# Optimization experiments

Measured on AMD Instinct MI355X. Metric: run time of the kernel, lower is better.

Reference implementation:

```python
import jax, jax.numpy as jnp
import numpy as np

C = 384; H = 32; W = 32; HEADS = 12; HD = C // HEADS; MLP = 1536
KOFF = 5; OFF_RANGE = 2.0


def layer_norm(x, g, b, eps=1e-5):
    mu = jnp.mean(x, axis=-1, keepdims=True)
    var = jnp.mean(jnp.square(x - mu), axis=-1, keepdims=True)
    return (x - mu) * jax.lax.rsqrt(var + eps) * g + b


def depthwise_conv(x, k):
    # x: (B,H,W,C), k: (kh,kw,1,C), SAME padding, groups=C
    return jax.lax.conv_general_dilated(
        x, k, window_strides=(1, 1), padding='SAME',
        dimension_numbers=('NHWC', 'HWIO', 'NHWC'), feature_group_count=C)


def grid_sample_bilinear(img, pos):
    # img: (B,H,W,C); pos: (B,H,W,2) normalized (y,x) in [-1,1], align_corners=True, border clamp
    B, Hh, Ww, Cc = img.shape
    py = (pos[..., 0] + 1.0) * 0.5 * (Hh - 1)
    px = (pos[..., 1] + 1.0) * 0.5 * (Ww - 1)
    y0 = jnp.floor(py); x0 = jnp.floor(px)
    wy = (py - y0)[..., None]; wx = (px - x0)[..., None]
    y0i = jnp.clip(y0.astype(jnp.int32), 0, Hh - 1)
    y1i = jnp.clip(y0i + 1, 0, Hh - 1)
    x0i = jnp.clip(x0.astype(jnp.int32), 0, Ww - 1)
    x1i = jnp.clip(x0i + 1, 0, Ww - 1)
    b = jnp.arange(B)[:, None, None]
    g = lambda yi, xi: img[b, yi, xi]
    return (g(y0i, x0i) * (1 - wy) * (1 - wx) + g(y0i, x1i) * (1 - wy) * wx
            + g(y1i, x0i) * wy * (1 - wx) + g(y1i, x1i) * wy * wx)


def setup_inputs() -> dict:
    key = jax.random.key(0)
    ks = jax.random.split(key, 16)
    n = jax.random.normal
    s = 0.02
    inp = {
        'x': n(ks[0], (16, H * W, C), jnp.float32),
        'ln1_g': jnp.ones((C,), jnp.float32), 'ln1_b': jnp.zeros((C,), jnp.float32),
        'Wq': n(ks[1], (C, C), jnp.float32) * s, 'bq': jnp.zeros((C,), jnp.float32),
        'off_k': n(ks[2], (KOFF, KOFF, 1, C), jnp.float32) * s,
        'off_kb': jnp.zeros((C,), jnp.float32),
        'offln_g': jnp.ones((C,), jnp.float32), 'offln_b': jnp.zeros((C,), jnp.float32),
        'Woff': n(ks[3], (2, C), jnp.float32) * s, 'boff': jnp.zeros((2,), jnp.float32),
        'Wk': n(ks[4], (C, C), jnp.float32) * s, 'bk': jnp.zeros((C,), jnp.float32),
        'Wv': n(ks[5], (C, C), jnp.float32) * s, 'bv': jnp.zeros((C,), jnp.float32),
        'Wo': n(ks[6], (C, C), jnp.float32) * s, 'bo': jnp.zeros((C,), jnp.float32),
        'ln2_g': jnp.ones((C,), jnp.float32), 'ln2_b': jnp.zeros((C,), jnp.float32),
        'W1': n(ks[7], (MLP, C), jnp.float32) * s, 'b1': jnp.zeros((MLP,), jnp.float32),
        'W2': n(ks[8], (C, MLP), jnp.float32) * s, 'b2': jnp.zeros((C,), jnp.float32),
    }
    return inp


def _block(x, ln1_g, ln1_b, Wq, bq, off_k, off_kb, offln_g, offln_b, Woff, boff,
           Wk, bk, Wv, bv, Wo, bo, ln2_g, ln2_b, W1, b1, W2, b2):
    B, N, _ = x.shape
    # --- deformable attention branch ---
    xn = layer_norm(x, ln1_g, ln1_b)
    xi = xn.reshape(B, H, W, C)
    q = xi @ Wq.T + bq                                  # (B,H,W,C)
    # offset network: depthwise conv -> LN -> GELU -> 1x1 conv to 2
    off = depthwise_conv(q, off_k) + off_kb
    off = jax.nn.gelu(layer_norm(off, offln_g, offln_b))
    off = off @ Woff.T + boff                           # (B,H,W,2)
    off_range = jnp.array([OFF_RANGE * 2.0 / H, OFF_RANGE * 2.0 / W], jnp.float32)
    off = jnp.tanh(off) * off_range                     # normalized coord units
    ry = (jnp.arange(H, dtype=jnp.float32) + 0.5) / H * 2.0 - 1.0
    rx = (jnp.arange(W, dtype=jnp.float32) + 0.5) / W * 2.0 - 1.0
    ref = jnp.stack(jnp.meshgrid(ry, rx, indexing='ij'), axis=-1)  # (H,W,2)
    pos = ref[None] + off                               # (B,H,W,2)
    xs = grid_sample_bilinear(xi, pos).reshape(B, N, C)  # sampled keys/values source
    k = xs @ Wk.T + bk
    v = xs @ Wv.T + bv
    qh = q.reshape(B, N, HEADS, HD).transpose(0, 2, 1, 3)
    kh = k.reshape(B, N, HEADS, HD).transpose(0, 2, 1, 3)
    vh = v.reshape(B, N, HEADS, HD).transpose(0, 2, 1, 3)
    attn = jax.nn.softmax(jnp.einsum('bhqd,bhkd->bhqk', qh, kh) * (HD ** -0.5), axis=-1)
    o = jnp.einsum('bhqk,bhkd->bhqd', attn, vh).transpose(0, 2, 1, 3).reshape(B, N, C)
    x = x + (o @ Wo.T + bo)
    # --- MLP branch ---
    y = layer_norm(x, ln2_g, ln2_b)
    y = jax.nn.gelu(y @ W1.T + b1) @ W2.T + b2
    return x + y


def reference(x, ln1_g, ln1_b, Wq, bq, off_k, off_kb, offln_g, offln_b, Woff, boff,
              Wk, bk, Wv, bv, Wo, bo, ln2_g, ln2_b, W1, b1, W2, b2):
    return _block(x, ln1_g, ln1_b, Wq, bq, off_k, off_kb, offln_g, offln_b, Woff, boff,
                  Wk, bk, Wv, bv, Wo, bo, ln2_g, ln2_b, W1, b1, W2, b2)
```

## Files before the change

kernel.cpp:

```cpp
#include <hip/hip_runtime.h>
#include <math.h>

#define DI __device__ __forceinline__

typedef __attribute__((ext_vector_type(8))) short bf16x8;
typedef __attribute__((ext_vector_type(4))) float f32x4;

static constexpr int CC = 384;
static constexpr float QSCALE = 0.17677669529663687f * 1.4426950408889634f;
static constexpr float INVQS  = 1.0f / QSCALE;

DI unsigned short f2bf(float f){
  unsigned u = __float_as_uint(f);
  u += 0x7FFFu + ((u >> 16) & 1u);
  return (unsigned short)(u >> 16);
}
DI float bf2f(unsigned short u){ return __uint_as_float((unsigned)u << 16); }
DI float lo16(unsigned u){ return __uint_as_float(u << 16); }
DI float hi16(unsigned u){ return __uint_as_float(u & 0xFFFF0000u); }
DI float fexp2(float x){ return __builtin_amdgcn_exp2f(x); }
DI float frcp(float x){ return __builtin_amdgcn_rcpf(x); }
DI float tanh_fast(float z){ return 1.f - 2.f*frcp(fexp2(2.8853900817779268f*z) + 1.f); }
DI float gelu_fast(float v){
  float u = v*v;
  float z = 0.7978845608028654f * fmaf(0.044715f*u, v, v);
  return v - v*frcp(fexp2(2.8853900817779268f*z) + 1.f);
}
DI f32x4 mfma16(bf16x8 a, bf16x8 b, f32x4 c){
  return __builtin_amdgcn_mfma_f32_16x16x32_bf16(a, b, c, 0, 0, 0);
}
DI void gload16(const unsigned short* g, unsigned short* l){
  __builtin_amdgcn_global_load_lds(
      (const __attribute__((address_space(1))) unsigned int*)(const void*)g,
      (__attribute__((address_space(3))) unsigned int*)(void*)l, 16, 0, 0);
}

__global__ __launch_bounds__(256) void k_cvt_all(
    const float* __restrict__ wq, const float* __restrict__ wk,
    const float* __restrict__ wv, const float* __restrict__ wo,
    const float* __restrict__ w1, const float* __restrict__ w2,
    const float* __restrict__ ofk,
    unsigned short* __restrict__ dst)
{
  int i4 = (blockIdx.x*256 + threadIdx.x)*4;
  if (i4 >= 1779072) return;
  const float* src; int off;
  if (i4 < 147456){ src = wq; off = i4; }
  else if (i4 < 294912){ src = wk; off = i4 - 147456; }
  else if (i4 < 442368){ src = wv; off = i4 - 294912; }
  else if (i4 < 589824){ src = wo; off = i4 - 442368; }
  else if (i4 < 1179648){ src = w1; off = i4 - 589824; }
  else if (i4 < 1769472){ src = w2; off = i4 - 1179648; }
  else { src = ofk; off = i4 - 1769472; }
  float4 v = *(const float4*)(src + off);
  uint2 o;
  o.x = ((unsigned)f2bf(v.y) << 16) | f2bf(v.x);
  o.y = ((unsigned)f2bf(v.w) << 16) | f2bf(v.z);
  *(uint2*)(dst + i4) = o;
}

template<int BIN>
__global__ __launch_bounds__(256) void k_ln(const float* __restrict__ xf,
    const unsigned short* __restrict__ xb,
    const float* __restrict__ g, const float* __restrict__ b,
    unsigned short* __restrict__ outb)
{
  int row = blockIdx.x*4 + (threadIdx.x >> 6);
  int l = threadIdx.x & 63;
  float v[6]; int ch[6];
  if constexpr (BIN){
    int cA = 4*l, cB = 256 + 2*l;
    ch[0]=cA; ch[1]=cA+1; ch[2]=cA+2; ch[3]=cA+3; ch[4]=cB; ch[5]=cB+1;
    const unsigned short* xp = xb + (size_t)row * CC;
    uint2 u2 = *(const uint2*)(xp + cA);
    unsigned u1 = *(const unsigned*)(xp + cB);
    v[0]=lo16(u2.x); v[1]=hi16(u2.x); v[2]=lo16(u2.y); v[3]=hi16(u2.y);
    v[4]=lo16(u1);   v[5]=hi16(u1);
  } else {
    const float* xp = xf + (size_t)row * CC;
#pragma unroll
    for (int p = 0; p < 6; p++){ ch[p] = l + 64*p; v[p] = xp[ch[p]]; }
  }
  float s = 0.f, s2 = 0.f;
#pragma unroll
  for (int p = 0; p < 6; p++){ s += v[p]; s2 += v[p]*v[p]; }
#pragma unroll
  for (int m = 32; m; m >>= 1){ s += __shfl_xor(s, m); s2 += __shfl_xor(s2, m); }
  float mu = s * (1.f/CC);
  float var = s2 * (1.f/CC) - mu*mu;
  float rs = rsqrtf(var + 1e-5f);
  float o[6];
#pragma unroll
  for (int p = 0; p < 6; p++) o[p] = (v[p] - mu) * rs * g[ch[p]] + b[ch[p]];
  unsigned short* op = outb + (size_t)row*CC;
  if constexpr (BIN){
    uint2 st;
    st.x = ((unsigned)f2bf(o[1]) << 16) | f2bf(o[0]);
    st.y = ((unsigned)f2bf(o[3]) << 16) | f2bf(o[2]);
    *(uint2*)(op + ch[0]) = st;
    *(unsigned*)(op + ch[4]) = ((unsigned)f2bf(o[5]) << 16) | f2bf(o[4]);
  } else {
#pragma unroll
    for (int p = 0; p < 6; p++) op[ch[p]] = f2bf(o[p]);
  }
}

template<int EPI>
__global__ __launch_bounds__(256) void k_gemm64(
    const unsigned short* __restrict__ A, const unsigned short* __restrict__ W,
    const float* __restrict__ bias, const float* __restrict__ bias2,
    const float* __restrict__ res, const unsigned short* __restrict__ resb,
    float* __restrict__ outf, unsigned short* __restrict__ outb,
    unsigned short* __restrict__ outb2, int ntn, int N, int K)
{
  __shared__ unsigned short As[2][2048];
  __shared__ unsigned short Bs[2][4096];
  int bid = blockIdx.x;
  int cpx = gridDim.x >> 3;
  int id = (bid & 7)*cpx + (bid >> 3);
  int bn = (id % ntn) * 128;
  int bm = (id / ntn) * 64;
  int t = threadIdx.x;
  int w = t >> 6, l = t & 63;
  int g = l >> 4, ln = l & 15;
  int wm = w >> 1, wn = w & 1;
  f32x4 acc[2][4];
#pragma unroll
  for (int i = 0; i < 2; i++)
#pragma unroll
    for (int j = 0; j < 4; j++) acc[i][j] = (f32x4){0.f,0.f,0.f,0.f};
  int srow = t >> 2, slot = t & 3;
  int srowB = srow + 64;
  int cb0 = (slot ^ (srow  & 3) ^ ((srow  >> 2) & 3)) * 8;
  int cb1 = (slot ^ (srowB & 3) ^ ((srowB >> 2) & 3)) * 8;
  const unsigned short* Ap  = A + (size_t)(bm + srow)*K + cb0;
  const unsigned short* Wp0 = W + (size_t)(bn + srow)*K + cb0;
  const unsigned short* Wp1 = W + (size_t)(bn + srowB)*K + cb1;
  int NT = K >> 5;
  int wl = w*512;
  gload16(Ap,  &As[0][wl]);
  gload16(Wp0, &Bs[0][wl]);
  gload16(Wp1, &Bs[0][wl + 2048]);
  __syncthreads();
  for (int kt = 0; kt < NT; kt++){
    int cur = kt & 1;
    if (kt + 1 < NT){
      int k0 = (kt + 1) << 5;
      gload16(Ap  + k0, &As[cur ^ 1][wl]);
      gload16(Wp0 + k0, &Bs[cur ^ 1][wl]);
      gload16(Wp1 + k0, &Bs[cur ^ 1][wl + 2048]);
    }
    bf16x8 af[2], bf[4];
#pragma unroll
    for (int mi = 0; mi < 2; mi++){
      int row = wm*32 + mi*16 + ln;
      int sl = g ^ (row & 3) ^ ((row >> 2) & 3);
      af[mi] = *(const bf16x8*)((const char*)As[cur] + row*64 + sl*16);
    }
#pragma unroll
    for (int ni = 0; ni < 4; ni++){
      int row = wn*64 + ni*16 + ln;
      int sl = g ^ (row & 3) ^ ((row >> 2) & 3);
      bf[ni] = *(const bf16x8*)((const char*)Bs[cur] + row*64 + sl*16);
    }
#pragma unroll
    for (int mi = 0; mi < 2; mi++)
#pragma unroll
      for (int ni = 0; ni < 4; ni++)
        acc[mi][ni] = mfma16(af[mi], bf[ni], acc[mi][ni]);
    if (kt + 1 < NT) __syncthreads();
  }
#pragma unroll
  for (int mi = 0; mi < 2; mi++)
#pragma unroll
  for (int ni = 0; ni < 4; ni++){
    int col = bn + wn*64 + ni*16 + ln;
    float bv;
    if constexpr (EPI == 6) bv = col < 384 ? bias[col] : bias2[col - 384];
    else bv = bias[col];
#pragma unroll
    for (int i = 0; i < 4; i++){
      int row = bm + wm*32 + mi*16 + g*4 + i;
      float v = acc[mi][ni][i] + bv;
      if constexpr (EPI == 2){ v += res[(size_t)row*N + col]; outb[(size_t)row*N + col] = f2bf(v); }
      if constexpr (EPI == 7){ v += bf2f(resb[(size_t)row*N + col]); outf[(size_t)row*N + col] = v; }
      if constexpr (EPI == 3) v = gelu_fast(v);
      if constexpr (EPI == 0) outf[(size_t)row*N + col] = v;
      if constexpr (EPI == 1 || EPI == 3) outb[(size_t)row*N + col] = f2bf(v);
      if constexpr (EPI == 5) outb[(size_t)row*N + col] = f2bf(v * QSCALE);
      if constexpr (EPI == 6){
        if (col < 384){
          outb[(size_t)row*384 + col] = f2bf(v);
        } else {
          int c = col - 384;
          int bb = row >> 10, key = row & 1023, h = c >> 5, d = c & 31;
          int k6 = key & 63;
          int phys = (key & ~63) | ((k6 & 15) << 2) | (k6 >> 4);
          outb2[(size_t)(((bb*12 + h) << 5) + d)*1024 + phys] = f2bf(v);
        }
      }
    }
  }
}

__global__ __launch_bounds__(256) void k_mlp1(
    const unsigned short* __restrict__ A, const unsigned short* __restrict__ W,
    const float* __restrict__ bias, unsigned short* __restrict__ outb)
{
  __shared__ unsigned short As[2][4096];
  __shared__ unsigned short Bs[2][4096];
  int bid = blockIdx.x;
  int cpx = gridDim.x >> 3;
  int id = (bid & 7)*cpx + (bid >> 3);
  int bn = (id % 12) * 128;
  int bm = (id / 12) * 128;
  int t = threadIdx.x;
  int w = t >> 6, l = t & 63;
  int g = l >> 4, ln = l & 15;
  int wm = w >> 1, wn = w & 1;
  f32x4 acc[4][4];
#pragma unroll
  for (int i = 0; i < 4; i++)
#pragma unroll
    for (int j = 0; j < 4; j++) acc[i][j] = (f32x4){0.f,0.f,0.f,0.f};
  int srow0 = t >> 2, slot = t & 3;
  int srow1 = srow0 + 64;
  int cb0 = (slot ^ (srow0 & 3) ^ ((srow0 >> 2) & 3)) * 8;
  int cb1 = (slot ^ (srow1 & 3) ^ ((srow1 >> 2) & 3)) * 8;
  const unsigned short* Ap0 = A + (size_t)(bm + srow0)*384 + cb0;
  const unsigned short* Ap1 = A + (size_t)(bm + srow1)*384 + cb1;
  const unsigned short* Wp0 = W + (size_t)(bn + srow0)*384 + cb0;
  const unsigned short* Wp1 = W + (size_t)(bn + srow1)*384 + cb1;
  int wl = w*512;
  gload16(Ap0, &As[0][wl]);
  gload16(Ap1, &As[0][wl + 2048]);
  gload16(Wp0, &Bs[0][wl]);
  gload16(Wp1, &Bs[0][wl + 2048]);
  __syncthreads();
  for (int kt = 0; kt < 12; kt++){
    int cur = kt & 1;
    if (kt < 11){
      int k0 = (kt + 1) << 5;
      gload16(Ap0 + k0, &As[cur ^ 1][wl]);
      gload16(Ap1 + k0, &As[cur ^ 1][wl + 2048]);
      gload16(Wp0 + k0, &Bs[cur ^ 1][wl]);
      gload16(Wp1 + k0, &Bs[cur ^ 1][wl + 2048]);
    }
    bf16x8 af[4], bf[4];
#pragma unroll
    for (int mi = 0; mi < 4; mi++){
      int row = wm*64 + mi*16 + ln;
      int sl = g ^ (row & 3) ^ ((row >> 2) & 3);
      af[mi] = *(const bf16x8*)((const char*)As[cur] + row*64 + sl*16);
    }
#pragma unroll
    for (int ni = 0; ni < 4; ni++){
      int row = wn*64 + ni*16 + ln;
      int sl = g ^ (row & 3) ^ ((row >> 2) & 3);
      bf[ni] = *(const bf16x8*)((const char*)Bs[cur] + row*64 + sl*16);
    }
#pragma unroll
    for (int mi = 0; mi < 4; mi++)
#pragma unroll
      for (int ni = 0; ni < 4; ni++)
        acc[mi][ni] = mfma16(af[mi], bf[ni], acc[mi][ni]);
    if (kt < 11) __syncthreads();
  }
#pragma unroll
  for (int mi = 0; mi < 4; mi++)
#pragma unroll
  for (int ni = 0; ni < 4; ni++){
    int col = bn + wn*64 + ni*16 + ln;
    float bv = bias[col];
#pragma unroll
    for (int i = 0; i < 4; i++){
      int row = bm + wm*64 + mi*16 + g*4 + i;
      float v = gelu_fast(acc[mi][ni][i] + bv);
      outb[(size_t)row*1536 + col] = f2bf(v);
    }
  }
}

__global__ __launch_bounds__(64) void k_offset_sample(
    const unsigned short* __restrict__ qs, const unsigned short* __restrict__ xnb,
    const unsigned short* __restrict__ okb,
    const float* __restrict__ offkb,
    const float* __restrict__ offg, const float* __restrict__ offb,
    const float* __restrict__ Woff, const float* __restrict__ boff,
    unsigned short* __restrict__ xsb)
{
  int blk = blockIdx.x;
  int pix = (blk & 7)*2048 + (blk >> 3);
  int b = pix >> 10, n = pix & 1023;
  int y = n >> 5, x = n & 31;
  int t = threadIdx.x;
  int c8 = (t < 48 ? t : 47) * 8;
  float act = t < 48 ? 1.f : 0.f;
  const unsigned short* qb = qs + (size_t)b*1024*CC;
  int ry[5], rx[5]; unsigned my[5], mx[5];
#pragma unroll
  for (int k = 0; k < 5; k++){
    int yy = y + k - 2, xx = x + k - 2;
    my[k] = (yy >= 0 && yy < 32) ? 0xFFFFFFFFu : 0u;
    mx[k] = (xx >= 0 && xx < 32) ? 0xFFFFFFFFu : 0u;
    int yc = yy < 0 ? 0 : (yy > 31 ? 31 : yy);
    int xc = xx < 0 ? 0 : (xx > 31 ? 31 : xx);
    ry[k] = yc*32*CC; rx[k] = xc*CC;
  }
  float a[8];
#pragma unroll
  for (int j = 0; j < 8; j++) a[j] = 0.f;
#pragma unroll
  for (int ky = 0; ky < 5; ky++)
#pragma unroll
  for (int kx = 0; kx < 5; kx++){
    int tap = ky*5 + kx;
    unsigned m = my[ky] & mx[kx];
    uint4 q4 = *(const uint4*)(qb + ry[ky] + rx[kx] + c8);
    uint4 w4 = *(const uint4*)(okb + tap*CC + c8);
    q4.x &= m; q4.y &= m; q4.z &= m; q4.w &= m;
    a[0] = fmaf(lo16(q4.x), lo16(w4.x), a[0]);
    a[1] = fmaf(hi16(q4.x), hi16(w4.x), a[1]);
    a[2] = fmaf(lo16(q4.y), lo16(w4.y), a[2]);
    a[3] = fmaf(hi16(q4.y), hi16(w4.y), a[3]);
    a[4] = fmaf(lo16(q4.z), lo16(w4.z), a[4]);
    a[5] = fmaf(hi16(q4.z), hi16(w4.z), a[5]);
    a[6] = fmaf(lo16(q4.w), lo16(w4.w), a[6]);
    a[7] = fmaf(hi16(q4.w), hi16(w4.w), a[7]);
  }
  float4 kbA = *(const float4*)(offkb + c8);
  float4 kbB = *(const float4*)(offkb + c8 + 4);
  float c[8];
  c[0] = act * fmaf(a[0], INVQS, kbA.x);
  c[1] = act * fmaf(a[1], INVQS, kbA.y);
  c[2] = act * fmaf(a[2], INVQS, kbA.z);
  c[3] = act * fmaf(a[3], INVQS, kbA.w);
  c[4] = act * fmaf(a[4], INVQS, kbB.x);
  c[5] = act * fmaf(a[5], INVQS, kbB.y);
  c[6] = act * fmaf(a[6], INVQS, kbB.z);
  c[7] = act * fmaf(a[7], INVQS, kbB.w);
  float s = 0.f, s2 = 0.f;
#pragma unroll
  for (int j = 0; j < 8; j++){ s += c[j]; s2 += c[j]*c[j]; }
#pragma unroll
  for (int m2 = 32; m2; m2 >>= 1){ s += __shfl_xor(s, m2); s2 += __shfl_xor(s2, m2); }
  float mu = s * (1.f/CC);
  float var = s2 * (1.f/CC) - mu*mu;
  float rs = rsqrtf(var + 1e-5f);
  float4 gA = *(const float4*)(offg + c8); float4 gB = *(const float4*)(offg + c8 + 4);
  float4 oA = *(const float4*)(offb + c8); float4 oB = *(const float4*)(offb + c8 + 4);
  float4 wA = *(const float4*)(Woff + c8); float4 wB = *(const float4*)(Woff + c8 + 4);
  float4 wC = *(const float4*)(Woff + CC + c8); float4 wD = *(const float4*)(Woff + CC + c8 + 4);
  float gg[8] = {gA.x,gA.y,gA.z,gA.w,gB.x,gB.y,gB.z,gB.w};
  float bb[8] = {oA.x,oA.y,oA.z,oA.w,oB.x,oB.y,oB.z,oB.w};
  float w0[8] = {wA.x,wA.y,wA.z,wA.w,wB.x,wB.y,wB.z,wB.w};
  float w1[8] = {wC.x,wC.y,wC.z,wC.w,wD.x,wD.y,wD.z,wD.w};
  float p0 = 0.f, p1 = 0.f;
#pragma unroll
  for (int j = 0; j < 8; j++){
    float v = gelu_fast((c[j] - mu)*rs*gg[j] + bb[j]) * act;
    p0 = fmaf(v, w0[j], p0);
    p1 = fmaf(v, w1[j], p1);
  }
#pragma unroll
  for (int m2 = 32; m2; m2 >>= 1){ p0 += __shfl_xor(p0, m2); p1 += __shfl_xor(p1, m2); }
  float offy = tanh_fast(p0 + boff[0]) * 0.125f;
  float offx = tanh_fast(p1 + boff[1]) * 0.125f;
  float py = ((y + 0.5f)/16.f - 1.f + offy + 1.f) * 0.5f * 31.f;
  float px = ((x + 0.5f)/16.f - 1.f + offx + 1.f) * 0.5f * 31.f;
  float y0f = floorf(py), x0f = floorf(px);
  float wy = py - y0f, wx = px - x0f;
  int y0 = (int)y0f, x0 = (int)x0f;
  y0 = y0 < 0 ? 0 : (y0 > 31 ? 31 : y0);
  x0 = x0 < 0 ? 0 : (x0 > 31 ? 31 : x0);
  int y1 = y0 + 1 > 31 ? 31 : y0 + 1;
  int x1 = x0 + 1 > 31 ? 31 : x0 + 1;
  const unsigned short* s00 = xnb + (size_t)(b*1024 + y0*32 + x0)*CC + c8;
  const unsigned short* s01 = xnb + (size_t)(b*1024 + y0*32 + x1)*CC + c8;
  const unsigned short* s10 = xnb + (size_t)(b*1024 + y1*32 + x0)*CC + c8;
  const unsigned short* s11 = xnb + (size_t)(b*1024 + y1*32 + x1)*CC + c8;
  float w00 = (1.f-wy)*(1.f-wx), w01 = (1.f-wy)*wx, w10 = wy*(1.f-wx), w11 = wy*wx;
  uint4 A0 = *(const uint4*)s00;
  uint4 A1 = *(const uint4*)s01;
  uint4 A2 = *(const uint4*)s10;
  uint4 A3 = *(const uint4*)s11;
  if (t < 48){
    float r[8];
    r[0] = w00*lo16(A0.x) + w01*lo16(A1.x) + w10*lo16(A2.x) + w11*lo16(A3.x);
    r[1] = w00*hi16(A0.x) + w01*hi16(A1.x) + w10*hi16(A2.x) + w11*hi16(A3.x);
    r[2] = w00*lo16(A0.y) + w01*lo16(A1.y) + w10*lo16(A2.y) + w11*lo16(A3.y);
    r[3] = w00*hi16(A0.y) + w01*hi16(A1.y) + w10*hi16(A2.y) + w11*hi16(A3.y);
    r[4] = w00*lo16(A0.z) + w01*lo16(A1.z) + w10*lo16(A2.z) + w11*lo16(A3.z);
    r[5] = w00*hi16(A0.z) + w01*hi16(A1.z) + w10*hi16(A2.z) + w11*hi16(A3.z);
    r[6] = w00*lo16(A0.w) + w01*lo16(A1.w) + w10*lo16(A2.w) + w11*lo16(A3.w);
    r[7] = w00*hi16(A0.w) + w01*hi16(A1.w) + w10*hi16(A2.w) + w11*hi16(A3.w);
    uint4 st;
    st.x = ((unsigned)f2bf(r[1]) << 16) | f2bf(r[0]);
    st.y = ((unsigned)f2bf(r[3]) << 16) | f2bf(r[2]);
    st.z = ((unsigned)f2bf(r[5]) << 16) | f2bf(r[4]);
    st.w = ((unsigned)f2bf(r[7]) << 16) | f2bf(r[6]);
    *(uint4*)(xsb + (size_t)(b*1024 + n)*CC + c8) = st;
  }
}

__global__ __launch_bounds__(256) void k_attn(
    const unsigned short* __restrict__ qs, const unsigned short* __restrict__ kb,
    const unsigned short* __restrict__ vt, unsigned short* __restrict__ ob)
{
  __shared__ unsigned short Ks[2][64][40];
  __shared__ unsigned short Vs[2][32][72];
  __shared__ unsigned short Ps[4][32][72];
  int blk = blockIdx.x;
  int sw = (blk & 7)*192 + (blk >> 3);
  int qt = sw & 7, h = (sw >> 3) % 12, b = sw / 96;
  int t = threadIdx.x;
  int w = t >> 6, l = t & 63;
  int g = l >> 4, ln = l & 15;
  int q0 = qt*128 + w*32;
  bf16x8 qa[2];
#pragma unroll
  for (int mi = 0; mi < 2; mi++)
    qa[mi] = *(const bf16x8*)&qs[(size_t)(b*1024 + q0 + mi*16 + ln)*CC + h*32 + g*8];
  bf16x8 vones;
#pragma unroll
  for (int j = 0; j < 8; j++) vones[j] = (short)0x3F80;
  f32x4 z = {0.f,0.f,0.f,0.f};
  f32x4 oacc[2][2]; oacc[0][0]=z; oacc[0][1]=z; oacc[1][0]=z; oacc[1][1]=z;
  f32x4 lacc[2]; lacc[0]=z; lacc[1]=z;
  int krow = t >> 2, kc = (t & 3)*8;
  int vdim = t >> 3, vc = (t & 7)*8;
  const unsigned short* kptr = kb + (size_t)(b*1024 + krow)*CC + h*32 + kc;
  const unsigned short* vptr = vt + (size_t)((b*12 + h)*32 + vdim)*1024 + vc;
  {
    uint4 kr = *(const uint4*)kptr;
    uint4 vr = *(const uint4*)vptr;
    *(uint4*)&Ks[0][krow][kc] = kr;
    *(uint4*)&Vs[0][vdim][vc] = vr;
  }
  __syncthreads();
  for (int kt = 0; kt < 16; kt++){
    int cur = kt & 1;
    uint4 kr2, vr2;
    if (kt < 15){
      int k0 = (kt + 1)*64;
      kr2 = *(const uint4*)(kptr + (size_t)k0*CC);
      vr2 = *(const uint4*)(vptr + k0);
    }
    bf16x8 kf[4];
#pragma unroll
    for (int nt = 0; nt < 4; nt++) kf[nt] = *(const bf16x8*)&Ks[cur][nt*16 + ln][g*8];
    f32x4 s[2][4];
    __builtin_amdgcn_s_setprio(1);
#pragma unroll
    for (int mi = 0; mi < 2; mi++)
#pragma unroll
      for (int nt = 0; nt < 4; nt++) s[mi][nt] = mfma16(qa[mi], kf[nt], z);
    __builtin_amdgcn_s_setprio(0);
#pragma unroll
    for (int mi = 0; mi < 2; mi++)
#pragma unroll
      for (int i = 0; i < 4; i++){
        float p0 = fexp2(s[mi][0][i]);
        float p1 = fexp2(s[mi][1][i]);
        float p2 = fexp2(s[mi][2][i]);
        float p3 = fexp2(s[mi][3][i]);
        int prow = mi*16 + g*4 + i;
        uint2 pk;
        pk.x = __builtin_amdgcn_perm(__float_as_uint(p1), __float_as_uint(p0), 0x07060302u);
        pk.y = __builtin_amdgcn_perm(__float_as_uint(p3), __float_as_uint(p2), 0x07060302u);
        *(uint2*)&Ps[w][prow][ln*4] = pk;
      }
    __builtin_amdgcn_s_setprio(1);
#pragma unroll
    for (int k2 = 0; k2 < 2; k2++){
      bf16x8 va[2];
#pragma unroll
      for (int d2 = 0; d2 < 2; d2++) va[d2] = *(const bf16x8*)&Vs[cur][d2*16 + ln][k2*32 + g*8];
#pragma unroll
      for (int mi = 0; mi < 2; mi++){
        bf16x8 pf = *(const bf16x8*)&Ps[w][mi*16 + ln][k2*32 + g*8];
#pragma unroll
        for (int d2 = 0; d2 < 2; d2++) oacc[mi][d2] = mfma16(pf, va[d2], oacc[mi][d2]);
        lacc[mi] = mfma16(pf, vones, lacc[mi]);
      }
    }
    __builtin_amdgcn_s_setprio(0);
    if (kt < 15){
      *(uint4*)&Ks[cur ^ 1][krow][kc] = kr2;
      *(uint4*)&Vs[cur ^ 1][vdim][vc] = vr2;
      __syncthreads();
    }
  }
  float rinv[2][4];
#pragma unroll
  for (int mi = 0; mi < 2; mi++)
#pragma unroll
    for (int i = 0; i < 4; i++) rinv[mi][i] = frcp(lacc[mi][i]);
#pragma unroll
  for (int mi = 0; mi < 2; mi++)
#pragma unroll
  for (int d2 = 0; d2 < 2; d2++)
#pragma unroll
  for (int i = 0; i < 4; i++){
    float v = oacc[mi][d2][i] * rinv[mi][i];
    int row = q0 + mi*16 + g*4 + i;
    ob[(size_t)(b*1024 + row)*CC + h*32 + d2*16 + ln] = f2bf(v);
  }
}

extern "C" void kernel_launch(void* const* d_in, const int* in_sizes, int n_in,
                              void* d_out, int out_size, void* d_ws, size_t ws_size,
                              hipStream_t stream)
{
  (void)in_sizes; (void)n_in; (void)out_size; (void)ws_size;
  const float* x     = (const float*)d_in[0];
  const float* ln1g  = (const float*)d_in[1];
  const float* ln1b  = (const float*)d_in[2];
  const float* Wq    = (const float*)d_in[3];
  const float* bq    = (const float*)d_in[4];
  const float* offk  = (const float*)d_in[5];
  const float* offkb = (const float*)d_in[6];
  const float* offg  = (const float*)d_in[7];
  const float* offb  = (const float*)d_in[8];
  const float* Woff  = (const float*)d_in[9];
  const float* boff  = (const float*)d_in[10];
  const float* Wk    = (const float*)d_in[11];
  const float* bk    = (const float*)d_in[12];
  const float* Wv    = (const float*)d_in[13];
  const float* bv    = (const float*)d_in[14];
  const float* Wo    = (const float*)d_in[15];
  const float* bo    = (const float*)d_in[16];
  const float* ln2g  = (const float*)d_in[17];
  const float* ln2b  = (const float*)d_in[18];
  const float* W1    = (const float*)d_in[19];
  const float* b1    = (const float*)d_in[20];
  const float* W2    = (const float*)d_in[21];
  const float* b2    = (const float*)d_in[22];

  char* ws = (char*)d_ws;
  unsigned short* X2B = (unsigned short*)ws;
  unsigned short* XSB = (unsigned short*)(ws + 25165824);
  unsigned short* KB  = (unsigned short*)(ws + 37748736);
  unsigned short* VT  = (unsigned short*)(ws + 50331648);
  unsigned short* OB  = (unsigned short*)(ws + 62914560);
  unsigned short* XNB = (unsigned short*)(ws + 75497472);
  unsigned short* QSB = (unsigned short*)(ws + 88080384);
  unsigned short* YB  = QSB;
  unsigned short* HB  = (unsigned short*)(ws + 25165824);
  unsigned short* WQB = (unsigned short*)(ws + 100663296);
  unsigned short* WKB = WQB + 147456;
  unsigned short* WOB = WKB + 294912;
  unsigned short* W1B = WOB + 147456;
  unsigned short* W2B = W1B + 589824;
  unsigned short* OKB = W2B + 589824;

  k_cvt_all<<<1738, 256, 0, stream>>>(Wq, Wk, Wv, Wo, W1, W2, offk, WQB);
  k_ln<0><<<4096, 256, 0, stream>>>(x, nullptr, ln1g, ln1b, XNB);
  k_gemm64<5><<<768, 256, 0, stream>>>(XNB, WQB, bq, nullptr, nullptr, nullptr, nullptr, QSB, nullptr, 3, 384, 384);
  k_offset_sample<<<16384, 64, 0, stream>>>(QSB, XNB, OKB, offkb, offg, offb, Woff, boff, XSB);
  k_gemm64<6><<<1536, 256, 0, stream>>>(XSB, WKB, bk, bv, nullptr, nullptr, nullptr, KB, VT, 6, 768, 384);
  k_attn<<<1536, 256, 0, stream>>>(QSB, KB, VT, OB);
  k_gemm64<2><<<768, 256, 0, stream>>>(OB, WOB, bo, nullptr, x, nullptr, nullptr, X2B, nullptr, 3, 384, 384);
  k_ln<1><<<4096, 256, 0, stream>>>(nullptr, X2B, ln2g, ln2b, YB);
  k_mlp1<<<1536, 256, 0, stream>>>(YB, W1B, b1, HB);
  k_gemm64<7><<<768, 256, 0, stream>>>(HB, W2B, b2, nullptr, nullptr, X2B, (float*)d_out, nullptr, nullptr, 3, 384, 1536);
}
```

Baseline: 240.3 us.

## Keep attention probabilities in registers via transposed QK^T MFMA

The score MFMA now runs with operands swapped, computing S^T. Each lane's accumulator then already matches the A-operand layout of the PV MFMA, so the exponentiated probabilities are packed to bf16 in registers instead of round-tripping through a per-warp shared-memory P buffer. The V-transpose permutation written by the QKV projection epilogue is changed to match the new key ordering within each 64-key tile. This removes LDS stores and loads and their latency, and frees shared memory, at the cost of tying correctness to that key permutation.

```diff
diff --git a/kernel.cpp b/kernel.cpp
--- a/kernel.cpp
+++ b/kernel.cpp
@@ -33,6 +33,9 @@
   __builtin_amdgcn_global_load_lds(
       (const __attribute__((address_space(1))) unsigned int*)(const void*)g,
       (__attribute__((address_space(3))) unsigned int*)(void*)l, 16, 0, 0);
+}
+DI unsigned packbf(float pa, float pb){
+  return __builtin_amdgcn_perm(__float_as_uint(pb), __float_as_uint(pa), 0x07060302u);
 }
 
 __global__ __launch_bounds__(256) void k_cvt_all(
@@ -195,7 +198,7 @@
           int c = col - 384;
           int bb = row >> 10, key = row & 1023, h = c >> 5, d = c & 31;
           int k6 = key & 63;
-          int phys = (key & ~63) | ((k6 & 15) << 2) | (k6 >> 4);
+          int phys = (key & ~63) | (k6 & 0x23) | ((k6 & 0xC) << 1) | ((k6 & 0x10) >> 2);
           outb2[(size_t)(((bb*12 + h) << 5) + d)*1024 + phys] = f2bf(v);
         }
       }
@@ -409,7 +412,6 @@
 {
   __shared__ unsigned short Ks[2][64][40];
   __shared__ unsigned short Vs[2][32][72];
-  __shared__ unsigned short Ps[4][32][72];
   int blk = blockIdx.x;
   int sw = (blk & 7)*192 + (blk >> 3);
   int qt = sw & 7, h = (sw >> 3) % 12, b = sw / 96;
@@ -449,27 +451,30 @@
     bf16x8 kf[4];
 #pragma unroll
     for (int nt = 0; nt < 4; nt++) kf[nt] = *(const bf16x8*)&Ks[cur][nt*16 + ln][g*8];
-    f32x4 s[2][4];
+    f32x4 st[2][4];
     __builtin_amdgcn_s_setprio(1);
 #pragma unroll
     for (int mi = 0; mi < 2; mi++)
 #pragma unroll
-      for (int nt = 0; nt < 4; nt++) s[mi][nt] = mfma16(qa[mi], kf[nt], z);
+      for (int nt = 0; nt < 4; nt++) st[mi][nt] = mfma16(kf[nt], qa[mi], z);
     __builtin_amdgcn_s_setprio(0);
-#pragma unroll
-    for (int mi = 0; mi < 2; mi++)
-#pragma unroll
-      for (int i = 0; i < 4; i++){
-        float p0 = fexp2(s[mi][0][i]);
-        float p1 = fexp2(s[mi][1][i]);
-        float p2 = fexp2(s[mi][2][i]);
-        float p3 = fexp2(s[mi][3][i]);
-        int prow = mi*16 + g*4 + i;
-        uint2 pk;
-        pk.x = __builtin_amdgcn_perm(__float_as_uint(p1), __float_as_uint(p0), 0x07060302u);
-        pk.y = __builtin_amdgcn_perm(__float_as_uint(p3), __float_as_uint(p2), 0x07060302u);
-        *(uint2*)&Ps[w][prow][ln*4] = pk;
+    bf16x8 pa[2][2];
+#pragma unroll
+    for (int mi = 0; mi < 2; mi++){
+#pragma unroll
+      for (int k2 = 0; k2 < 2; k2++){
+        float e0 = fexp2(st[mi][2*k2][0]),   e1 = fexp2(st[mi][2*k2][1]);
+        float e2 = fexp2(st[mi][2*k2][2]),   e3 = fexp2(st[mi][2*k2][3]);
+        float f0 = fexp2(st[mi][2*k2+1][0]), f1 = fexp2(st[mi][2*k2+1][1]);
+        float f2 = fexp2(st[mi][2*k2+1][2]), f3 = fexp2(st[mi][2*k2+1][3]);
+        uint4 pw;
+        pw.x = packbf(e0, e1);
+        pw.y = packbf(e2, e3);
+        pw.z = packbf(f0, f1);
+        pw.w = packbf(f2, f3);
+        pa[mi][k2] = *(bf16x8*)&pw;
       }
+    }
     __builtin_amdgcn_s_setprio(1);
 #pragma unroll
     for (int k2 = 0; k2 < 2; k2++){
@@ -478,10 +483,9 @@
       for (int d2 = 0; d2 < 2; d2++) va[d2] = *(const bf16x8*)&Vs[cur][d2*16 + ln][k2*32 + g*8];
 #pragma unroll
       for (int mi = 0; mi < 2; mi++){
-        bf16x8 pf = *(const bf16x8*)&Ps[w][mi*16 + ln][k2*32 + g*8];
-#pragma unroll
-        for (int d2 = 0; d2 < 2; d2++) oacc[mi][d2] = mfma16(pf, va[d2], oacc[mi][d2]);
-        lacc[mi] = mfma16(pf, vones, lacc[mi]);
+#pragma unroll
+        for (int d2 = 0; d2 < 2; d2++) oacc[mi][d2] = mfma16(pa[mi][k2], va[d2], oacc[mi][d2]);
+        lacc[mi] = mfma16(pa[mi][k2], vones, lacc[mi]);
       }
     }
     __builtin_amdgcn_s_setprio(0);
```

After: 235.3 us. 2.1% less time.
